# Kernel tuning notes

Hardware: AMD Instinct MI355X
Metric: run time of the kernel (lower is better)

Reference implementation:

```python
import jax, jax.numpy as jnp
import numpy as np

SFREQ = 250.0
L_FREQ, H_FREQ = 4.0, 8.0
N_TAPS = 413  # odd, zero-phase FIR


def _bandpass_fir(numtaps, lf, hf, sfreq):
    # Hamming-windowed sinc band-pass (firwin-style), matching MNE's fir_design='firwin' spirit
    n = np.arange(numtaps) - (numtaps - 1) / 2.0
    lp = lambda fc: (2.0 * fc / sfreq) * np.sinc(2.0 * fc / sfreq * n)
    h = (lp(hf) - lp(lf)) * np.hamming(numtaps)
    return h.astype(np.float32)


def setup_inputs() -> dict:
    key = jax.random.key(0)
    x = jax.random.normal(key, (64, 64, 10000), dtype=jnp.float32)
    h = jnp.asarray(_bandpass_fir(N_TAPS, L_FREQ, H_FREQ, SFREQ))
    return {"x": x, "h": h}


def reference(x, h):
    # x: [B, C, T], h: [n_h] FIR filter. Equivalent math to _overlap_add_filter:
    # reflect_limited padding + full linear FFT convolution + zero-phase crop.
    T = x.shape[-1]
    n_h = h.shape[0]
    n_edge = min(n_h, T) - 1
    # reflect_limited pad: 2*x[0] - x[n_edge:0:-1] (left), 2*x[-1] - x[-2:-n_edge-2:-1] (right)
    left = 2.0 * x[..., :1] - x[..., 1:n_edge + 1][..., ::-1]
    right = 2.0 * x[..., -1:] - x[..., -n_edge - 1:-1][..., ::-1]
    x_ext = jnp.concatenate([left, x, right], axis=-1)  # [B, C, T + 2*n_edge]
    n_x = T + 2 * n_edge
    n_full = n_x + n_h - 1
    n_fft = 1 << (n_full - 1).bit_length()  # single big FFT == overlap-add result
    Xf = jnp.fft.rfft(x_ext, n_fft)
    Hf = jnp.fft.rfft(h.astype(x_ext.dtype), n_fft)
    y = jnp.fft.irfft(Xf * Hf, n_fft)  # full linear convolution of x_ext with h
    shift = (n_h - 1) // 2 + n_edge  # zero-phase delay compensation + edge crop
    return jax.lax.dynamic_slice_in_dim(y, shift, T, axis=-1).astype(x.dtype)
```

## Files before the change

### kernel.cpp

```cpp
#include <hip/hip_runtime.h>


#define T_LEN 10000
#define N_H   413
#define SHIFT 206
#define TB    576
#define SPAN  1024
#define SPANP 1032
#define NQ    14
#define NTBLK 18

typedef _Float16 v8h   __attribute__((ext_vector_type(8)));
typedef float    v4f   __attribute__((ext_vector_type(4)));
typedef float    f32x2 __attribute__((ext_vector_type(2)));

__global__ __launch_bounds__(256, 3) void FilterBank_20624432955781_kernel(
    const float* __restrict__ x, const float* __restrict__ h, float* __restrict__ out) {
    __shared__ _Float16 lds_e[16][SPANP];
    __shared__ _Float16 gqh[464], gql[464];

    const int tid = threadIdx.x;
    const int t0b = blockIdx.x * TB;
    const int r0  = blockIdx.y * 16;
    const float* __restrict__ xblk = x + (size_t)r0 * T_LEN;

    for (int z = tid; z < 464; z += 256) {
        const float gv = (z >= 15 && z < 15 + N_H) ? h[427 - z] : 0.0f;
        const _Float16 hi = (_Float16)gv;
        gqh[z] = hi;
        gql[z] = (_Float16)(gv - (float)hi);
    }

    for (int gidx = tid; gidx < 16 * (SPAN / 8); gidx += 256) {
        const int rr = gidx >> 7;
        const int c8 = gidx & 127;
        const int j0 = t0b + c8 * 8;
        const float* __restrict__ xr = xblk + (size_t)rr * T_LEN;
        float v[8];
        if (j0 >= SHIFT && j0 + 8 <= T_LEN + SHIFT) {
            const f32x2* xp = (const f32x2*)(xr + (j0 - SHIFT));
            #pragma unroll
            for (int p = 0; p < 4; ++p) { f32x2 t2 = xp[p]; v[2*p] = t2.x; v[2*p+1] = t2.y; }
        } else {
            #pragma unroll
            for (int k = 0; k < 8; ++k) {
                const int j = j0 + k;
                if (j < SHIFT)              v[k] = 2.0f * xr[0] - xr[SHIFT - j];
                else if (j < T_LEN + SHIFT) v[k] = xr[j - SHIFT];
                else                        v[k] = 2.0f * xr[T_LEN - 1] - xr[2 * T_LEN + SHIFT - 2 - j];
            }
        }
        v8h hv;
        #pragma unroll
        for (int k = 0; k < 8; ++k) hv[k] = (_Float16)v[k];
        *(v8h*)&lds_e[rr][c8 * 8] = hv;
    }
    __syncthreads();

    const int l   = tid & 63;
    const int wv  = tid >> 6;
    const int g4  = l >> 4;
    const int r16 = l & 15;

    v8h afh[NQ], afl[NQ];
    #pragma unroll
    for (int q = 0; q < NQ; ++q) {
        const int zb = 32 * q + 8 * g4 - r16 + 15;
        #pragma unroll
        for (int i = 0; i < 8; ++i) { afh[q][i] = gqh[zb + i]; afl[q][i] = gql[zb + i]; }
    }

    const int NT = (min(TB, T_LEN - t0b)) >> 4;
    for (int tt = wv; tt < NT; tt += 4) {
        const int trel = tt * 16;
        const v8h* __restrict__ bp = (const v8h*)&lds_e[r16][trel + 8 * g4];
        v4f acc0 = {0.f, 0.f, 0.f, 0.f};
        v4f acc1 = {0.f, 0.f, 0.f, 0.f};
        #pragma unroll
        for (int q = 0; q < NQ; ++q) {
            const v8h b = bp[4 * q];
            acc0 = __builtin_amdgcn_mfma_f32_16x16x32_f16(afh[q], b, acc0, 0, 0, 0);
            acc1 = __builtin_amdgcn_mfma_f32_16x16x32_f16(afl[q], b, acc1, 0, 0, 0);
        }
        const v4f acc = acc0 + acc1;
        float* op = out + (size_t)(r0 + r16) * T_LEN + (t0b + trel + 4 * g4);
        *(v4f*)op = acc;
    }
}

extern "C" void kernel_launch(void* const* d_in, const int* in_sizes, int n_in,
                              void* d_out, int out_size, void* d_ws, size_t ws_size,
                              hipStream_t stream) {
    const float* x = (const float*)d_in[0];
    const float* h = (const float*)d_in[1];
    float* out = (float*)d_out;
    dim3 grid(NTBLK, 64 * 64 / 16);
    FilterBank_20624432955781_kernel<<<grid, dim3(256), 0, stream>>>(x, h, out);
}
```

Baseline: 371.7 us.

## Switch FIR Toeplitz-MFMA to 32x32x16 tiles with swizzled LDS and row-major filter reuse

```diff
diff --git a/kernel.cpp b/kernel.cpp
--- a/kernel.cpp
+++ b/kernel.cpp
@@ -4,88 +4,119 @@
 #define T_LEN 10000
 #define N_H   413
 #define SHIFT 206
-#define TB    576
-#define SPAN  1024
-#define SPANP 1032
-#define NQ    14
-#define NTBLK 18
+#define CB    320
+#define NSEG  32
+#define NSLOT 96
+#define ROWH  (NSLOT * 8)
+#define NQ    28
+#define AROWL 472
 
 typedef _Float16 v8h   __attribute__((ext_vector_type(8)));
+typedef float    v16f  __attribute__((ext_vector_type(16)));
 typedef float    v4f   __attribute__((ext_vector_type(4)));
 typedef float    f32x2 __attribute__((ext_vector_type(2)));
 
-__global__ __launch_bounds__(256, 3) void FilterBank_20624432955781_kernel(
+template <int NT>
+__device__ __forceinline__ void compute_tiles(
+    const _Float16* __restrict__ lds_e, const _Float16* __restrict__ a0,
+    const _Float16* __restrict__ a1, float* __restrict__ out,
+    int t0b, int r0, int tbeg, int l) {
+    const int n   = l & 31;
+    const int hh  = l >> 5;
+    const int vv0 = 24 + 8 * hh - 8 * (n >> 3);
+    const v8h* __restrict__ pah = (const v8h*)(a0 + (n & 7) * AROWL + vv0);
+    const v8h* __restrict__ pal = (const v8h*)(a1 + (n & 7) * AROWL + vv0);
+    const char* __restrict__ eb = (const char*)lds_e + n * (ROWH * 2);
+    const int nx = n & 7;
+
+    v16f acc[NT];
+    #pragma unroll
+    for (int t = 0; t < NT; ++t) acc[t] = (v16f)(0.0f);
+
+    #pragma unroll
+    for (int q = 0; q < NQ; ++q) {
+        const v8h ah = pah[2 * q];
+        const v8h al = pal[2 * q];
+        #pragma unroll
+        for (int t = 0; t < NT; ++t) {
+            const int s = 4 * (tbeg + t) + hh + 2 * q;
+            const v8h b = *(const v8h*)(eb + ((s ^ nx) << 4));
+            acc[t] = __builtin_amdgcn_mfma_f32_32x32x16_f16(ah, b, acc[t], 0, 0, 0);
+            acc[t] = __builtin_amdgcn_mfma_f32_32x32x16_f16(al, b, acc[t], 0, 0, 0);
+        }
+    }
+
+    #pragma unroll
+    for (int t = 0; t < NT; ++t) {
+        const int tt = tbeg + t;
+        float* __restrict__ orow =
+            out + (size_t)(r0 + n) * T_LEN + (t0b + 32 * tt + 4 * hh);
+        #pragma unroll
+        for (int g = 0; g < 4; ++g) {
+            const int tg = t0b + 32 * tt + 8 * g + 4 * hh;
+            if (tg < T_LEN) {
+                *(v4f*)(orow + 8 * g) =
+                    (v4f){acc[t][4*g], acc[t][4*g+1], acc[t][4*g+2], acc[t][4*g+3]};
+            }
+        }
+    }
+}
+
+__global__ __launch_bounds__(256, 2) void FilterBank_20624432955781_kernel(
     const float* __restrict__ x, const float* __restrict__ h, float* __restrict__ out) {
-    __shared__ _Float16 lds_e[16][SPANP];
-    __shared__ _Float16 gqh[464], gql[464];
+    __shared__ alignas(16) _Float16 lds_e[32 * ROWH];
+    __shared__ alignas(16) _Float16 arow[2][8][AROWL];
 
     const int tid = threadIdx.x;
-    const int t0b = blockIdx.x * TB;
-    const int r0  = blockIdx.y * 16;
-    const float* __restrict__ xblk = x + (size_t)r0 * T_LEN;
+    const int t0b = blockIdx.x * CB;
+    const int r0  = blockIdx.y * 32;
 
-    for (int z = tid; z < 464; z += 256) {
-        const float gv = (z >= 15 && z < 15 + N_H) ? h[427 - z] : 0.0f;
+    for (int z = tid; z < 8 * AROWL; z += 256) {
+        const int r = z / AROWL, vv = z - r * AROWL;
+        const int idx = 436 + r - vv;
+        const float gv = (idx >= 0 && idx < N_H) ? h[idx] : 0.0f;
         const _Float16 hi = (_Float16)gv;
-        gqh[z] = hi;
-        gql[z] = (_Float16)(gv - (float)hi);
+        arow[0][r][vv] = hi;
+        arow[1][r][vv] = (_Float16)(gv - (float)hi);
     }
 
-    for (int gidx = tid; gidx < 16 * (SPAN / 8); gidx += 256) {
-        const int rr = gidx >> 7;
-        const int c8 = gidx & 127;
-        const int j0 = t0b + c8 * 8;
-        const float* __restrict__ xr = xblk + (size_t)rr * T_LEN;
-        float v[8];
-        if (j0 >= SHIFT && j0 + 8 <= T_LEN + SHIFT) {
-            const f32x2* xp = (const f32x2*)(xr + (j0 - SHIFT));
+    {
+        const int rr = tid >> 3;
+        const float* __restrict__ xr = x + (size_t)(r0 + rr) * T_LEN;
+        _Float16* __restrict__ erow = lds_e + rr * ROWH;
+        const int rx = rr & 7;
+        #pragma unroll
+        for (int it = 0; it < 12; ++it) {
+            const int c8 = (tid & 7) + 8 * it;
+            const int j0 = t0b + c8 * 8;
+            float v[8];
+            if (j0 >= SHIFT && j0 + 8 <= T_LEN + SHIFT) {
+                const f32x2* xp = (const f32x2*)(xr + (j0 - SHIFT));
+                #pragma unroll
+                for (int p = 0; p < 4; ++p) { f32x2 t2 = xp[p]; v[2*p] = t2.x; v[2*p+1] = t2.y; }
+            } else {
+                #pragma unroll
+                for (int k = 0; k < 8; ++k) {
+                    const int j = j0 + k;
+                    if (j < SHIFT)              v[k] = 2.0f * xr[0] - xr[SHIFT - j];
+                    else if (j < T_LEN + SHIFT) v[k] = xr[j - SHIFT];
+                    else                        v[k] = 2.0f * xr[T_LEN - 1] - xr[2 * T_LEN + SHIFT - 2 - j];
+                }
+            }
+            v8h hv;
             #pragma unroll
-            for (int p = 0; p < 4; ++p) { f32x2 t2 = xp[p]; v[2*p] = t2.x; v[2*p+1] = t2.y; }
-        } else {
-            #pragma unroll
-            for (int k = 0; k < 8; ++k) {
-                const int j = j0 + k;
-                if (j < SHIFT)              v[k] = 2.0f * xr[0] - xr[SHIFT - j];
-                else if (j < T_LEN + SHIFT) v[k] = xr[j - SHIFT];
-                else                        v[k] = 2.0f * xr[T_LEN - 1] - xr[2 * T_LEN + SHIFT - 2 - j];
-            }
+            for (int k = 0; k < 8; ++k) hv[k] = (_Float16)v[k];
+            *(v8h*)(erow + ((c8 ^ rx) * 8)) = hv;
         }
-        v8h hv;
-        #pragma unroll
-        for (int k = 0; k < 8; ++k) hv[k] = (_Float16)v[k];
-        *(v8h*)&lds_e[rr][c8 * 8] = hv;
     }
     __syncthreads();
 
-    const int l   = tid & 63;
-    const int wv  = tid >> 6;
-    const int g4  = l >> 4;
-    const int r16 = l & 15;
-
-    v8h afh[NQ], afl[NQ];
-    #pragma unroll
-    for (int q = 0; q < NQ; ++q) {
-        const int zb = 32 * q + 8 * g4 - r16 + 15;
-        #pragma unroll
-        for (int i = 0; i < 8; ++i) { afh[q][i] = gqh[zb + i]; afl[q][i] = gql[zb + i]; }
-    }
-
-    const int NT = (min(TB, T_LEN - t0b)) >> 4;
-    for (int tt = wv; tt < NT; tt += 4) {
-        const int trel = tt * 16;
-        const v8h* __restrict__ bp = (const v8h*)&lds_e[r16][trel + 8 * g4];
-        v4f acc0 = {0.f, 0.f, 0.f, 0.f};
-        v4f acc1 = {0.f, 0.f, 0.f, 0.f};
-        #pragma unroll
-        for (int q = 0; q < NQ; ++q) {
-            const v8h b = bp[4 * q];
-            acc0 = __builtin_amdgcn_mfma_f32_16x16x32_f16(afh[q], b, acc0, 0, 0, 0);
-            acc1 = __builtin_amdgcn_mfma_f32_16x16x32_f16(afl[q], b, acc1, 0, 0, 0);
-        }
-        const v4f acc = acc0 + acc1;
-        float* op = out + (size_t)(r0 + r16) * T_LEN + (t0b + trel + 4 * g4);
-        *(v4f*)op = acc;
-    }
+    const int l  = tid & 63;
+    const int wv = tid >> 6;
+    const _Float16* a0 = &arow[0][0][0];
+    const _Float16* a1 = &arow[1][0][0];
+    if (wv < 2) compute_tiles<3>(lds_e, a0, a1, out, t0b, r0, 3 * wv, l);
+    else        compute_tiles<2>(lds_e, a0, a1, out, t0b, r0, 6 + 2 * (wv - 2), l);
 }
 
 extern "C" void kernel_launch(void* const* d_in, const int* in_sizes, int n_in,
@@ -94,6 +125,6 @@
     const float* x = (const float*)d_in[0];
     const float* h = (const float*)d_in[1];
     float* out = (float*)d_out;
-    dim3 grid(NTBLK, 64 * 64 / 16);
+    dim3 grid(NSEG, 64 * 64 / 32);
     FilterBank_20624432955781_kernel<<<grid, dim3(256), 0, stream>>>(x, h, out);
 }
```

Result: slower. 415.2 us (+11.7%).
